# Optimization experiments

Hardware: AMD Instinct MI355X
Metric: run time of the kernel (lower is better)

Reference implementation:

```python
import jax, jax.numpy as jnp
import numpy as np

B, N, C = 4, 4096, 768
H = 8
HD = C // H  # head_dim = 96
SCALE = HD ** -0.5
EPS = 1e-12  # torch F.normalize eps


def setup_inputs() -> dict:
    key = jax.random.key(0)
    ks = jax.random.split(key, 6)
    s = C ** -0.5
    return {
        "context_x": jax.random.normal(ks[0], (B, N, C), dtype=jnp.float32),
        "depth_x": jax.random.normal(ks[1], (B, N, C), dtype=jnp.float32),
        "Wq": jax.random.normal(ks[2], (C, C), dtype=jnp.float32) * s,
        "Wkv": jax.random.normal(ks[3], (C, 2 * C), dtype=jnp.float32) * s,
        "Wproj": jax.random.normal(ks[4], (C, C), dtype=jnp.float32) * s,
        "bproj": jax.random.normal(ks[5], (C,), dtype=jnp.float32) * 0.01,
    }


def _l2norm(x):
    # matches torch.nn.functional.normalize(x, dim=-1)
    n = jnp.sqrt(jnp.sum(x * x, axis=-1, keepdims=True))
    return x / jnp.maximum(n, EPS)


def reference(context_x, depth_x, Wq, Wkv, Wproj, bproj):
    b, n, c = context_x.shape
    # projections
    q = (context_x @ Wq).reshape(b, n, H, HD).transpose(0, 2, 3, 1)  # [B,H,hd,N]
    kv = (depth_x @ Wkv).reshape(b, n, 2, H, HD)
    k = kv[:, :, 0].transpose(0, 2, 3, 1)  # [B,H,hd,N]
    v = kv[:, :, 1].transpose(0, 2, 3, 1)  # [B,H,hd,N]
    # cosine-normalize over the token axis (last dim after transpose)
    q = _l2norm(q)
    k = _l2norm(k)
    # channel-attention (cross-covariance): attn is [B,H,hd,hd]
    attn = jnp.einsum("bhdn,bhen->bhde", q, k) * SCALE
    attn = jax.nn.softmax(attn, axis=-1)
    x = jnp.einsum("bhde,bhen->bhdn", attn, v)  # [B,H,hd,N]
    x = x.transpose(0, 3, 1, 2).reshape(b, n, c)  # [B,N,C]
    return x @ Wproj + bproj
```

## Files before the change

kernel.cpp:

```cpp
#include <hip/hip_runtime.h>


using bf16x8 = __attribute__((ext_vector_type(8))) short;
using f32x4  = __attribute__((ext_vector_type(4))) float;

#define SCALE_ 0.10206207261596575f
#define KD 768

__device__ __forceinline__ unsigned short f2bf(float f) {
    unsigned int u = __builtin_bit_cast(unsigned int, f);
    u += 0x7FFFu + ((u >> 16) & 1u);
    return (unsigned short)(u >> 16);
}
__device__ __forceinline__ float bf2f(unsigned short h) {
    unsigned int u = ((unsigned int)h) << 16;
    return __builtin_bit_cast(float, u);
}

__device__ __forceinline__ void glds16(const unsigned short* g, unsigned short* l) {
    __builtin_amdgcn_global_load_lds(
        (const __attribute__((address_space(1))) void*)g,
        (__attribute__((address_space(3))) void*)l, 16, 0, 0);
}

__device__ __forceinline__ float ssq8(bf16x8 v) {
    uint4 u = __builtin_bit_cast(uint4, v);
    unsigned a[4] = {u.x, u.y, u.z, u.w};
    float s = 0.f;
    #pragma unroll
    for (int i = 0; i < 4; i++) {
        float lo = __builtin_bit_cast(float, a[i] << 16);
        float hi = __builtin_bit_cast(float, a[i] & 0xFFFF0000u);
        s += lo * lo + hi * hi;
    }
    return s;
}

__global__ void prep_k(const float* __restrict__ ctx, unsigned short* __restrict__ ctxB,
                       const float* __restrict__ dep, unsigned short* __restrict__ depB,
                       const float* __restrict__ Wq, unsigned short* __restrict__ WqT,
                       const float* __restrict__ Wkv, unsigned short* __restrict__ WkvT,
                       const float* __restrict__ Wproj, unsigned short* __restrict__ WprojT)
{
    __shared__ float tile[32][33];
    int bid = blockIdx.x;
    if (bid < 12288) {
        const float* in; unsigned short* out;
        if (bid < 6144) { in = ctx; out = ctxB; }
        else            { in = dep; out = depB; bid -= 6144; }
        size_t idx = ((size_t)bid * 256 + threadIdx.x) * 8;
        float4 v0 = *(const float4*)&in[idx];
        float4 v1 = *(const float4*)&in[idx + 4];
        unsigned short h[8];
        h[0] = f2bf(v0.x); h[1] = f2bf(v0.y); h[2] = f2bf(v0.z); h[3] = f2bf(v0.w);
        h[4] = f2bf(v1.x); h[5] = f2bf(v1.y); h[6] = f2bf(v1.z); h[7] = f2bf(v1.w);
        *(bf16x8*)&out[idx] = *(bf16x8*)h;
        return;
    }
    bid -= 12288;
    const float* W; unsigned short* Wt; int N, bx, by;
    if (bid < 576)       { W = Wq;    Wt = WqT;    N = 768;  bx = bid % 24;  by = bid / 24; }
    else if (bid < 1728) { bid -= 576;  W = Wkv;   Wt = WkvT; N = 1536; bx = bid % 48;  by = bid / 48; }
    else                 { bid -= 1728; W = Wproj; Wt = WprojT; N = 768; bx = bid % 24;  by = bid / 24; }
    int n0 = bx * 32, k0 = by * 32;
    int tx = threadIdx.x & 31, ty = threadIdx.x >> 5;
    #pragma unroll
    for (int i = 0; i < 32; i += 8)
        tile[ty + i][tx] = W[(size_t)(k0 + ty + i) * N + n0 + tx];
    __syncthreads();
    #pragma unroll
    for (int i = 0; i < 32; i += 8)
        Wt[(size_t)(n0 + ty + i) * 768 + k0 + tx] = f2bf(tile[tx][ty + i]);
}


#define BAR __builtin_amdgcn_s_barrier()
#define VM(n) asm volatile("s_waitcnt vmcnt(" #n ")" ::: "memory")

#define ST_A(sbase, tt, h) do { \
    _Pragma("unroll") \
    for (int c_ = 0; c_ < 2; c_++) \
        glds16(gA + (size_t)(((h) * 8 + w) * 16) * KD + (tt) * 64 + c_ * 32, \
               (sbase) + (c_ * 16 + (h) * 8 + w) * 512); \
} while (0)

#define ST_B(sbase, tt) do { \
    _Pragma("unroll") \
    for (int c_ = 0; c_ < 2; c_++) \
        glds16(gB + (size_t)(w * 16) * KD + (tt) * 64 + c_ * 32, \
               (sbase) + (c_ * 8 + w) * 512); \
} while (0)

#define RD_A(cbase, mh) do { \
    _Pragma("unroll") \
    for (int i_ = 0; i_ < 2; i_++) \
    _Pragma("unroll") \
    for (int kk_ = 0; kk_ < 2; kk_++) \
        a[i_][kk_] = *(const bf16x8*)&(cbase)[(kk_ * 16 + wr * 4 + (mh) * 2 + i_) * 512 + lane * 8]; \
} while (0)

#define RD_B(cbase, nh) do { \
    _Pragma("unroll") \
    for (int j_ = 0; j_ < 2; j_++) \
    _Pragma("unroll") \
    for (int kk_ = 0; kk_ < 2; kk_++) \
        b[nh][j_][kk_] = *(const bf16x8*)&(cbase)[(kk_ * 8 + wc * 4 + (nh) * 2 + j_) * 512 + lane * 8]; \
} while (0)

#define MM(mh, nh) do { \
    _Pragma("unroll") \
    for (int i_ = 0; i_ < 2; i_++) \
    _Pragma("unroll") \
    for (int j_ = 0; j_ < 2; j_++) \
    _Pragma("unroll") \
    for (int kk_ = 0; kk_ < 2; kk_++) \
        acc[(mh) * 2 + i_][(nh) * 2 + j_] = __builtin_amdgcn_mfma_f32_16x16x32_bf16( \
            a[i_][kk_], b[nh][j_][kk_], acc[(mh) * 2 + i_][(nh) * 2 + j_], 0, 0, 0); \
} while (0)

#define KLOOP do { \
    { \
        unsigned short* a0 = S;                  unsigned short* b0 = S + 16384; \
        unsigned short* a1 = S + 24576;          unsigned short* b1 = S + 24576 + 16384; \
        ST_A(a0, 0, 0); ST_A(a0, 0, 1); ST_B(b0, 0); \
        ST_A(a1, 1, 0); ST_A(a1, 1, 1); ST_B(b1, 1); \
    } \
    VM(6); \
    BAR; \
    unsigned cur = 0; \
    for (int tt = 0; tt < 12; ++tt) { \
        unsigned short* cA = S + cur * 24576; \
        unsigned short* cB = cA + 16384; \
        unsigned sg = cur + 2; if (sg >= 3) sg -= 3; \
        unsigned short* sA = S + sg * 24576; \
        unsigned short* sB = sA + 16384; \
        const bool st = (tt <= 9); \
        RD_A(cA, 0); RD_B(cB, 0); if (st) ST_A(sA, tt + 2, 0); \
        BAR; MM(0, 0); BAR; \
        RD_B(cB, 1); if (st) ST_A(sA, tt + 2, 1); \
        BAR; MM(0, 1); BAR; \
        RD_A(cA, 1); if (st) ST_B(sB, tt + 2); \
        BAR; MM(1, 0); BAR; \
        MM(1, 1); \
        if (tt < 10) { VM(6); } \
        else if (tt == 10) { VM(0); } \
        BAR; \
        cur = cur + 1; if (cur == 3) cur = 0; \
    } \
} while (0)

__global__ __launch_bounds__(512, 2) void gemm_qkv(
    const unsigned short* __restrict__ ctxB, const unsigned short* __restrict__ WqT,
    const unsigned short* __restrict__ depB, const unsigned short* __restrict__ WkvT,
    unsigned short* __restrict__ Qt, unsigned short* __restrict__ Kt,
    unsigned short* __restrict__ Vb)
{
    __shared__ unsigned short S[3 * 24576];

    int bid = blockIdx.x;
    const bool isQ = (bid < 384);
    const unsigned short* A; const unsigned short* Bt; int lin;
    if (isQ) { A = ctxB; Bt = WqT;  lin = bid; }
    else     { A = depB; Bt = WkvT; lin = bid - 384; }

    const int xcd = lin & 7, li = lin >> 3;
    const int mt = xcd * 8 + (li & 7);
    const int nt = li >> 3;
    const int bm = mt * 256, bn = nt * 128;

    const int t = threadIdx.x, lane = t & 63, w = t >> 6;
    const int wr = w >> 1, wc = w & 1;
    const int mf = lane & 15, quad = lane >> 4;

    const unsigned short* gA = A  + (size_t)(bm + (lane & 15)) * KD + (lane >> 4) * 8;
    const unsigned short* gB = Bt + (size_t)(bn + (lane & 15)) * KD + (lane >> 4) * 8;

    f32x4 acc[4][4] = {};
    bf16x8 a[2][2], b[2][2][2];

    KLOOP;

    unsigned short* Tr = isQ ? Qt : Kt;
    const bool kpart = isQ || (bn < 768);
    #pragma unroll
    for (int i = 0; i < 4; i++) {
        int row0 = bm + wr * 64 + i * 16 + quad * 4;
        int bb = row0 >> 12, n = row0 & 4095;
        #pragma unroll
        for (int j = 0; j < 4; j++) {
            int c = bn + wc * 64 + j * 16 + mf;
            if (kpart) {
                int h = (c * 683) >> 16;
                int d = c - h * 96;
                size_t o = ((size_t)((bb * 8 + h) * 96 + d)) * 4096 + n;
                ushort4 v4;
                v4.x = f2bf(acc[i][j][0]); v4.y = f2bf(acc[i][j][1]);
                v4.z = f2bf(acc[i][j][2]); v4.w = f2bf(acc[i][j][3]);
                *(ushort4*)&Tr[o] = v4;
            } else {
                int cv = c - 768;
                #pragma unroll
                for (int r = 0; r < 4; r++)
                    Vb[(size_t)(row0 + r) * 768 + cv] = f2bf(acc[i][j][r]);
            }
        }
    }
}

__global__ __launch_bounds__(512, 2) void gemm_proj(
    const unsigned short* __restrict__ A, const unsigned short* __restrict__ Bt,
    const float* __restrict__ bias, float* __restrict__ C, int N)
{
    __shared__ unsigned short S[3 * 24576];

    const int Nt = gridDim.x, Mt = gridDim.y;
    const int lin = blockIdx.y * Nt + blockIdx.x;
    const int xcd = lin & 7, li = lin >> 3;
    const int band = Mt >> 3;
    const int mt = xcd * band + (li % band);
    const int nt = li / band;
    const int bm = mt * 256, bn = nt * 128;

    const int t = threadIdx.x, lane = t & 63, w = t >> 6;
    const int wr = w >> 1, wc = w & 1;
    const int mf = lane & 15, quad = lane >> 4;

    const unsigned short* gA = A  + (size_t)(bm + (lane & 15)) * KD + (lane >> 4) * 8;
    const unsigned short* gB = Bt + (size_t)(bn + (lane & 15)) * KD + (lane >> 4) * 8;

    f32x4 acc[4][4] = {};
    bf16x8 a[2][2], b[2][2][2];

    KLOOP;

    #pragma unroll
    for (int i = 0; i < 4; i++) {
        int row0 = bm + wr * 64 + i * 16 + quad * 4;
        #pragma unroll
        for (int j = 0; j < 4; j++) {
            int col = bn + wc * 64 + j * 16 + mf;
            float bv = bias[col];
            #pragma unroll
            for (int r = 0; r < 4; r++)
                C[(size_t)(row0 + r) * N + col] = acc[i][j][r] + bv;
        }
    }
}

#undef KLOOP
#undef MM
#undef RD_A
#undef RD_B
#undef ST_A
#undef ST_B
#undef VM
#undef BAR

__global__ __launch_bounds__(256) void s_gemm(
    const unsigned short* __restrict__ Qt, const unsigned short* __restrict__ Kt,
    float* __restrict__ Spart, float* __restrict__ ssq)
{
    __shared__ unsigned short Qs[2][12 * 512];
    __shared__ unsigned short Ks[2][12 * 512];
    const int s = blockIdx.x, bh = blockIdx.y;
    const int t = threadIdx.x, lane = t & 63, w = t >> 6;
    const int m0 = (w >> 1) * 48, n0w = (w & 1) * 48;
    const int mf = lane & 15, quad = lane >> 4;
    const int srow = lane & 15, skc = (lane >> 4) * 8;
    const int nwin = s * 512;

    const unsigned short* Qg = Qt + (size_t)bh * 96 * 4096;
    const unsigned short* Kg = Kt + (size_t)bh * 96 * 4096;

    f32x4 acc[3][3] = {};
    float sq[3] = {0.f, 0.f, 0.f}, sk[3] = {0.f, 0.f, 0.f};

    #pragma unroll
    for (int c = 0; c < 3; c++) {
        int bi = w * 3 + c, kc = bi / 6, g = bi % 6;
        size_t go = (size_t)(g * 16 + srow) * 4096 + nwin + kc * 32 + skc;
        glds16(Qg + go, &Qs[0][bi * 512]);
        glds16(Kg + go, &Ks[0][bi * 512]);
    }

    for (int it = 0; it < 8; it++) {
        const int cur = it & 1;
        __syncthreads();
        if (it + 1 < 8) {
            const int nxt = cur ^ 1;
            const int nn = nwin + (it + 1) * 64;
            #pragma unroll
            for (int c = 0; c < 3; c++) {
                int bi = w * 3 + c, kc = bi / 6, g = bi % 6;
                size_t go = (size_t)(g * 16 + srow) * 4096 + nn + kc * 32 + skc;
                glds16(Qg + go, &Qs[nxt][bi * 512]);
                glds16(Kg + go, &Ks[nxt][bi * 512]);
            }
        }
        #pragma unroll
        for (int kk = 0; kk < 2; kk++) {
            bf16x8 a[3], b[3];
            #pragma unroll
            for (int i = 0; i < 3; i++)
                a[i] = *(const bf16x8*)&Qs[cur][(kk * 6 + (w >> 1) * 3 + i) * 512 + lane * 8];
            #pragma unroll
            for (int j = 0; j < 3; j++)
                b[j] = *(const bf16x8*)&Ks[cur][(kk * 6 + (w & 1) * 3 + j) * 512 + lane * 8];
            if ((w & 1) == 0) {
                #pragma unroll
                for (int i = 0; i < 3; i++) sq[i] += ssq8(a[i]);
            }
            if ((w >> 1) == 0) {
                #pragma unroll
                for (int j = 0; j < 3; j++) sk[j] += ssq8(b[j]);
            }
            #pragma unroll
            for (int i = 0; i < 3; i++)
                #pragma unroll
                for (int j = 0; j < 3; j++)
                    acc[i][j] = __builtin_amdgcn_mfma_f32_16x16x32_bf16(a[i], b[j], acc[i][j], 0, 0, 0);
        }
    }

    if ((w & 1) == 0) {
        #pragma unroll
        for (int i = 0; i < 3; i++) {
            float v = sq[i];
            v += __shfl_xor(v, 16, 64);
            v += __shfl_xor(v, 32, 64);
            if (lane < 16) atomicAdd(&ssq[bh * 96 + m0 + i * 16 + lane], v);
        }
    }
    if ((w >> 1) == 0) {
        #pragma unroll
        for (int j = 0; j < 3; j++) {
            float v = sk[j];
            v += __shfl_xor(v, 16, 64);
            v += __shfl_xor(v, 32, 64);
            if (lane < 16) atomicAdd(&ssq[3072 + bh * 96 + n0w + j * 16 + lane], v);
        }
    }

    float* outp = Spart + (size_t)(bh * 8 + s) * 9216;
    #pragma unroll
    for (int i = 0; i < 3; i++)
        #pragma unroll
        for (int j = 0; j < 3; j++) {
            int e  = n0w + j * 16 + mf;
            int d0 = m0 + i * 16 + quad * 4;
            #pragma unroll
            for (int r = 0; r < 4; r++)
                outp[(d0 + r) * 96 + e] = acc[i][j][r];
        }
}

__global__ __launch_bounds__(256) void softmax_k(
    const float* __restrict__ Spart, const float* __restrict__ ssq,
    unsigned short* __restrict__ P)
{
    const int bh = blockIdx.y;
    const int d  = blockIdx.x * 4 + (threadIdx.x >> 6);
    const int lane = threadIdx.x & 63;

    const float sr = SCALE_ / fmaxf(sqrtf(ssq[bh * 96 + d]), 1e-12f);

    const float* Sp = Spart + (size_t)bh * 8 * 9216 + d * 96;
    float sa = 0.f, sb = 0.f;
    #pragma unroll
    for (int ch = 0; ch < 8; ch++) {
        sa += Sp[ch * 9216 + lane];
        if (lane < 32) sb += Sp[ch * 9216 + 64 + lane];
    }
    float ka = 1.0f / fmaxf(sqrtf(ssq[3072 + bh * 96 + lane]), 1e-12f);
    float va = sa * sr * ka;
    float vb = -1e30f;
    if (lane < 32) {
        float kb = 1.0f / fmaxf(sqrtf(ssq[3072 + bh * 96 + 64 + lane]), 1e-12f);
        vb = sb * sr * kb;
    }

    float m = fmaxf(va, vb);
    #pragma unroll
    for (int off = 32; off >= 1; off >>= 1)
        m = fmaxf(m, __shfl_xor(m, off, 64));

    float ea = __expf(va - m);
    float eb = (lane < 32) ? __expf(vb - m) : 0.f;
    float ssum = ea + eb;
    #pragma unroll
    for (int off = 32; off >= 1; off >>= 1)
        ssum += __shfl_xor(ssum, off, 64);

    float inv = 1.0f / ssum;
    unsigned short* Pr = P + (size_t)bh * 9216 + d * 96;
    Pr[lane] = f2bf(ea * inv);
    if (lane < 32) Pr[64 + lane] = f2bf(eb * inv);
}

__global__ __launch_bounds__(256) void pv_gemm(
    const unsigned short* __restrict__ Vb, const unsigned short* __restrict__ P,
    unsigned short* __restrict__ X)
{
    __shared__ unsigned short Ps[96][104];
    int ntile = blockIdx.x, bh = blockIdx.y;
    int b = bh >> 3, h = bh & 7;
    int t = threadIdx.x, lane = t & 63, w = t >> 6;

    const unsigned short* Pg = P + (size_t)bh * 9216;
    #pragma unroll
    for (int i = 0; i < 9; i++) {
        int idx4 = t + 256 * i;
        int row = idx4 / 24, c4 = (idx4 - row * 24) * 4;
        *(ushort4*)&Ps[row][c4] = *(const ushort4*)&Pg[row * 96 + c4];
    }
    __syncthreads();

    const unsigned short* Vbase = Vb + (size_t)b * 4096 * 768 + h * 96;
    int mf = lane & 15, k8 = (lane >> 4) * 8;
    f32x4 acc[2][6] = {};
    #pragma unroll
    for (int k = 0; k < 3; k++) {
        bf16x8 a[2], bb[6];
        #pragma unroll
        for (int i = 0; i < 2; i++) {
            int row = ntile * 128 + w * 32 + i * 16 + mf;
            a[i] = *(const bf16x8*)&Vbase[(size_t)row * 768 + k * 32 + k8];
        }
        #pragma unroll
        for (int j = 0; j < 6; j++)
            bb[j] = *(const bf16x8*)&Ps[j * 16 + mf][k * 32 + k8];
        #pragma unroll
        for (int i = 0; i < 2; i++)
            #pragma unroll
            for (int j = 0; j < 6; j++)
                acc[i][j] = __builtin_amdgcn_mfma_f32_16x16x32_bf16(a[i], bb[j], acc[i][j], 0, 0, 0);
    }
    #pragma unroll
    for (int i = 0; i < 2; i++)
        #pragma unroll
        for (int j = 0; j < 6; j++)
            #pragma unroll
            for (int r = 0; r < 4; r++) {
                int n_tok = ntile * 128 + w * 32 + i * 16 + (lane >> 4) * 4 + r;
                int c = h * 96 + j * 16 + mf;
                X[((size_t)b * 4096 + n_tok) * 768 + c] = f2bf(acc[i][j][r]);
            }
}

extern "C" void kernel_launch(void* const* d_in, const int* in_sizes, int n_in,
                              void* d_out, int out_size, void* d_ws, size_t ws_size,
                              hipStream_t stream)
{
    (void)in_sizes; (void)n_in; (void)out_size; (void)ws_size;
    const float* ctx   = (const float*)d_in[0];
    const float* dep   = (const float*)d_in[1];
    const float* Wq    = (const float*)d_in[2];
    const float* Wkv   = (const float*)d_in[3];
    const float* Wproj = (const float*)d_in[4];
    const float* bproj = (const float*)d_in[5];
    float* out = (float*)d_out;

    char* p = (char*)d_ws;
    auto carve = [&](size_t bytes) {
        char* r = p;
        p += (bytes + 255) & ~(size_t)255;
        return r;
    };
    unsigned short* WqT    = (unsigned short*)carve((size_t)768 * 768 * 2);
    unsigned short* WkvT   = (unsigned short*)carve((size_t)1536 * 768 * 2);
    unsigned short* WprojT = (unsigned short*)carve((size_t)768 * 768 * 2);
    unsigned short* Qt     = (unsigned short*)carve((size_t)32 * 96 * 4096 * 2);
    unsigned short* Kt     = (unsigned short*)carve((size_t)32 * 96 * 4096 * 2);
    unsigned short* Vb     = (unsigned short*)carve((size_t)16384 * 768 * 2);
    unsigned short* Xb     = (unsigned short*)carve((size_t)16384 * 768 * 2);
    float*          ssq    = (float*)carve((size_t)2 * 3072 * 4);
    float*          Spart  = (float*)carve((size_t)32 * 8 * 9216 * 4);
    unsigned short* Pb     = (unsigned short*)carve((size_t)32 * 9216 * 2);
    unsigned short* depB   = (unsigned short*)carve((size_t)16384 * 768 * 2);
    unsigned short* ctxB   = Xb;

    hipMemsetAsync(ssq, 0, 2 * 3072 * 4, stream);

    prep_k<<<14592, 256, 0, stream>>>(ctx, ctxB, dep, depB,
                                      Wq, WqT, Wkv, WkvT, Wproj, WprojT);

    gemm_qkv<<<1152, 512, 0, stream>>>(ctxB, WqT, depB, WkvT, Qt, Kt, Vb);

    s_gemm<<<dim3(8, 32), 256, 0, stream>>>(Qt, Kt, Spart, ssq);
    softmax_k<<<dim3(24, 32), 256, 0, stream>>>(Spart, ssq, Pb);
    pv_gemm<<<dim3(32, 32), 256, 0, stream>>>(Vb, Pb, Xb);
    gemm_proj<<<dim3(6, 64), 512, 0, stream>>>(Xb, WprojT, bproj, out, 768);
}
```

Baseline: 214.2 us.

## Fuse fp32-to-bf16 activation conversion into QKV GEMM register-staged loads

Removes the separate activation conversion pass from prep_k. The QKV GEMM now loads fp32 ctx/dep tiles straight into registers, converts them to bf16 and writes them to LDS, replacing the async global_load_lds path with a register-staged pipeline. This drops a full write and reread of the bf16 activation copies, about 50MB of traffic. In exchange, each A-tile global read doubles in size, more registers are needed (launch bounds lowered to 1 block per SM), and load latency hiding now depends on a manual software pipeline.

```diff
diff --git a/kernel.cpp b/kernel.cpp
--- a/kernel.cpp
+++ b/kernel.cpp
@@ -36,28 +36,12 @@
     return s;
 }
 
-__global__ void prep_k(const float* __restrict__ ctx, unsigned short* __restrict__ ctxB,
-                       const float* __restrict__ dep, unsigned short* __restrict__ depB,
-                       const float* __restrict__ Wq, unsigned short* __restrict__ WqT,
+__global__ void prep_k(const float* __restrict__ Wq, unsigned short* __restrict__ WqT,
                        const float* __restrict__ Wkv, unsigned short* __restrict__ WkvT,
                        const float* __restrict__ Wproj, unsigned short* __restrict__ WprojT)
 {
     __shared__ float tile[32][33];
     int bid = blockIdx.x;
-    if (bid < 12288) {
-        const float* in; unsigned short* out;
-        if (bid < 6144) { in = ctx; out = ctxB; }
-        else            { in = dep; out = depB; bid -= 6144; }
-        size_t idx = ((size_t)bid * 256 + threadIdx.x) * 8;
-        float4 v0 = *(const float4*)&in[idx];
-        float4 v1 = *(const float4*)&in[idx + 4];
-        unsigned short h[8];
-        h[0] = f2bf(v0.x); h[1] = f2bf(v0.y); h[2] = f2bf(v0.z); h[3] = f2bf(v0.w);
-        h[4] = f2bf(v1.x); h[5] = f2bf(v1.y); h[6] = f2bf(v1.z); h[7] = f2bf(v1.w);
-        *(bf16x8*)&out[idx] = *(bf16x8*)h;
-        return;
-    }
-    bid -= 12288;
     const float* W; unsigned short* Wt; int N, bx, by;
     if (bid < 576)       { W = Wq;    Wt = WqT;    N = 768;  bx = bid % 24;  by = bid / 24; }
     else if (bid < 1728) { bid -= 576;  W = Wkv;   Wt = WkvT; N = 1536; bx = bid % 48;  by = bid / 48; }
@@ -76,6 +60,7 @@
 
 #define BAR __builtin_amdgcn_s_barrier()
 #define VM(n) asm volatile("s_waitcnt vmcnt(" #n ")" ::: "memory")
+#define LGK0 asm volatile("s_waitcnt lgkmcnt(0)" ::: "memory")
 
 #define ST_A(sbase, tt, h) do { \
     _Pragma("unroll") \
@@ -116,6 +101,55 @@
     for (int kk_ = 0; kk_ < 2; kk_++) \
         acc[(mh) * 2 + i_][(nh) * 2 + j_] = __builtin_amdgcn_mfma_f32_16x16x32_bf16( \
             a[i_][kk_], b[nh][j_][kk_], acc[(mh) * 2 + i_][(nh) * 2 + j_], 0, 0, 0); \
+} while (0)
+
+#define LD_A(RA, tt) do { \
+    _Pragma("unroll") \
+    for (int q_ = 0; q_ < 4; q_++) { \
+        const float* ap_ = gAf + (size_t)(((q_ >> 1) * 8 + w) * 16) * KD + (tt) * 64 + (q_ & 1) * 32; \
+        RA[2 * q_]     = *(const float4*)ap_; \
+        RA[2 * q_ + 1] = *(const float4*)(ap_ + 4); \
+    } \
+} while (0)
+
+#define CVT_DSW(sbase, RA) do { \
+    _Pragma("unroll") \
+    for (int q_ = 0; q_ < 4; q_++) { \
+        unsigned short hh_[8]; \
+        float4 x0_ = RA[2 * q_], x1_ = RA[2 * q_ + 1]; \
+        hh_[0] = f2bf(x0_.x); hh_[1] = f2bf(x0_.y); hh_[2] = f2bf(x0_.z); hh_[3] = f2bf(x0_.w); \
+        hh_[4] = f2bf(x1_.x); hh_[5] = f2bf(x1_.y); hh_[6] = f2bf(x1_.z); hh_[7] = f2bf(x1_.w); \
+        *(bf16x8*)((sbase) + ((q_ & 1) * 16 + (q_ >> 1) * 8 + w) * 512 + lane * 8) = *(bf16x8*)hh_; \
+    } \
+} while (0)
+
+#define LD_B(RB, tt) do { \
+    _Pragma("unroll") \
+    for (int c_ = 0; c_ < 2; c_++) \
+        RB[c_] = *(const bf16x8*)(gB + (size_t)(w * 16) * KD + (tt) * 64 + c_ * 32); \
+} while (0)
+
+#define WR_B(sbase, RB) do { \
+    _Pragma("unroll") \
+    for (int c_ = 0; c_ < 2; c_++) \
+        *(bf16x8*)((sbase) + (c_ * 8 + w) * 512 + lane * 8) = RB[c_]; \
+} while (0)
+
+#define QTILE(tt, RBw, RBl) do { \
+    unsigned short* cA = S + cur * 24576; \
+    unsigned short* cB = cA + 16384; \
+    unsigned sg1 = cur + 1; if (sg1 >= 3) sg1 -= 3; \
+    unsigned short* sA1 = S + sg1 * 24576; \
+    unsigned short* sB1 = sA1 + 16384; \
+     RD_A(cA, 0); RD_B(cB, 0); if ((tt) < 11) LD_A(RA, (tt) + 1); \
+    BAR; MM(0, 0); BAR; \
+     RD_B(cB, 1); if ((tt) < 10) LD_B(RBl, (tt) + 2); \
+    BAR; MM(0, 1); BAR; \
+     RD_A(cA, 1); \
+    if ((tt) < 11) { CVT_DSW(sA1, RA); WR_B(sB1, RBw); LGK0; } \
+    BAR; MM(1, 0); BAR; \
+     MM(1, 1); BAR; \
+    cur = cur + 1; if (cur == 3) cur = 0; \
 } while (0)
 
 #define KLOOP do { \
@@ -149,9 +183,9 @@
     } \
 } while (0)
 
-__global__ __launch_bounds__(512, 2) void gemm_qkv(
-    const unsigned short* __restrict__ ctxB, const unsigned short* __restrict__ WqT,
-    const unsigned short* __restrict__ depB, const unsigned short* __restrict__ WkvT,
+__global__ __launch_bounds__(512, 1) void gemm_qkv(
+    const float* __restrict__ ctx, const unsigned short* __restrict__ WqT,
+    const float* __restrict__ dep, const unsigned short* __restrict__ WkvT,
     unsigned short* __restrict__ Qt, unsigned short* __restrict__ Kt,
     unsigned short* __restrict__ Vb)
 {
@@ -159,9 +193,9 @@
 
     int bid = blockIdx.x;
     const bool isQ = (bid < 384);
-    const unsigned short* A; const unsigned short* Bt; int lin;
-    if (isQ) { A = ctxB; Bt = WqT;  lin = bid; }
-    else     { A = depB; Bt = WkvT; lin = bid - 384; }
+    const float* Af; const unsigned short* Bt; int lin;
+    if (isQ) { Af = ctx; Bt = WqT;  lin = bid; }
+    else     { Af = dep; Bt = WkvT; lin = bid - 384; }
 
     const int xcd = lin & 7, li = lin >> 3;
     const int mt = xcd * 8 + (li & 7);
@@ -172,13 +206,26 @@
     const int wr = w >> 1, wc = w & 1;
     const int mf = lane & 15, quad = lane >> 4;
 
-    const unsigned short* gA = A  + (size_t)(bm + (lane & 15)) * KD + (lane >> 4) * 8;
-    const unsigned short* gB = Bt + (size_t)(bn + (lane & 15)) * KD + (lane >> 4) * 8;
+    const float*          gAf = Af + (size_t)(bm + (lane & 15)) * KD + (lane >> 4) * 8;
+    const unsigned short* gB  = Bt + (size_t)(bn + (lane & 15)) * KD + (lane >> 4) * 8;
 
     f32x4 acc[4][4] = {};
     bf16x8 a[2][2], b[2][2][2];
-
-    KLOOP;
+    float4 RA[8];
+    bf16x8 RBe[2], RBo[2];
+
+    LD_A(RA, 0); CVT_DSW(S, RA);
+    LD_B(RBe, 0); WR_B(S + 16384, RBe);
+    LD_B(RBo, 1);
+    LGK0;
+    BAR;
+
+    unsigned cur = 0;
+    #pragma unroll 1
+    for (int it = 0; it < 6; ++it) {
+        QTILE(2 * it,     RBo, RBe);
+        QTILE(2 * it + 1, RBe, RBo);
+    }
 
     unsigned short* Tr = isQ ? Qt : Kt;
     const bool kpart = isQ || (bn < 768);
@@ -247,15 +294,6 @@
     }
 }
 
-#undef KLOOP
-#undef MM
-#undef RD_A
-#undef RD_B
-#undef ST_A
-#undef ST_B
-#undef VM
-#undef BAR
-
 __global__ __launch_bounds__(256) void s_gemm(
     const unsigned short* __restrict__ Qt, const unsigned short* __restrict__ Kt,
     float* __restrict__ Spart, float* __restrict__ ssq)
@@ -476,15 +514,12 @@
     float*          ssq    = (float*)carve((size_t)2 * 3072 * 4);
     float*          Spart  = (float*)carve((size_t)32 * 8 * 9216 * 4);
     unsigned short* Pb     = (unsigned short*)carve((size_t)32 * 9216 * 2);
-    unsigned short* depB   = (unsigned short*)carve((size_t)16384 * 768 * 2);
-    unsigned short* ctxB   = Xb;
 
     hipMemsetAsync(ssq, 0, 2 * 3072 * 4, stream);
 
-    prep_k<<<14592, 256, 0, stream>>>(ctx, ctxB, dep, depB,
-                                      Wq, WqT, Wkv, WkvT, Wproj, WprojT);
-
-    gemm_qkv<<<1152, 512, 0, stream>>>(ctxB, WqT, depB, WkvT, Qt, Kt, Vb);
+    prep_k<<<2304, 256, 0, stream>>>(Wq, WqT, Wkv, WkvT, Wproj, WprojT);
+
+    gemm_qkv<<<1152, 512, 0, stream>>>(ctx, WqT, dep, WkvT, Qt, Kt, Vb);
 
     s_gemm<<<dim3(8, 32), 256, 0, stream>>>(Qt, Kt, Spart, ssq);
     softmax_k<<<dim3(24, 32), 256, 0, stream>>>(Spart, ssq, Pb);
```

Result: slower. 276.4 us (+29.1%).
